# Performance work log

Measured on AMD Instinct MI355X. Metric: run time of the kernel, lower is better.

The kernel has to match this reference:

```python
import jax, jax.numpy as jnp
import numpy as np

N = 768          # number of atoms
DIM = 3
F = 128          # feature width
N_RBF = 32       # gaussian radial basis size
CUTOFF = 5.0
NUM_CHAINS = 4
T_IN_K = 300.0
TTIME = 20.0
KB = 8.617330337217213e-05   # Boltzmann constant, eV/K (ASE units.kB)
BOX = 24.8                   # box side so that ~26 neighbors/atom within cutoff
GAMMA = 1.0 / (CUTOFF / N_RBF) ** 2  # RBF width


def setup_inputs() -> dict:
    key = jax.random.key(0)
    ks = jax.random.split(key, 12)
    q = jax.random.uniform(ks[0], (N, DIM), dtype=jnp.float32) * BOX
    v = jax.random.normal(ks[1], (N, DIM), dtype=jnp.float32) * 0.01
    p_eta = jax.random.normal(ks[2], (NUM_CHAINS,), dtype=jnp.float32) * 0.1
    mass = jax.random.uniform(ks[3], (N,), dtype=jnp.float32, minval=1.0, maxval=20.0)
    atomic_numbers = jax.random.randint(ks[4], (N,), 0, 100, dtype=jnp.int32)
    embed = jax.random.normal(ks[5], (100, F), dtype=jnp.float32) * 0.1
    W1 = jax.random.normal(ks[6], (N_RBF, F), dtype=jnp.float32) / np.sqrt(N_RBF)
    b1 = jnp.zeros((F,), dtype=jnp.float32)
    W2 = jax.random.normal(ks[7], (F, F), dtype=jnp.float32) / np.sqrt(F)
    b2 = jnp.zeros((F,), dtype=jnp.float32)
    W3 = jax.random.normal(ks[8], (F, F), dtype=jnp.float32) / np.sqrt(F)
    w_out = jax.random.normal(ks[9], (F,), dtype=jnp.float32) / np.sqrt(F)
    return dict(v=v, q=q, p_eta=p_eta, mass=mass, embed=embed, W1=W1, b1=b1,
                W2=W2, b2=b2, W3=W3, w_out=w_out, atomic_numbers=atomic_numbers)


def _energy(q, atomic_numbers, embed, W1, b1, W2, b2, W3, w_out):
    """SchNet-style cutoff-graph potential energy (scalar)."""
    h = embed[atomic_numbers]                                   # [N,F]
    disp = q[:, None, :] - q[None, :, :]                        # [N,N,3]
    d2 = jnp.sum(disp * disp, axis=-1)                          # [N,N]
    eye = jnp.eye(N, dtype=bool)
    mask = (d2 < CUTOFF ** 2) & (~eye)                          # cutoff neighbor list (dense mask)
    d = jnp.sqrt(jnp.where(mask, d2, 1.0))                      # safe sqrt off-graph
    centers = jnp.linspace(0.0, CUTOFF, N_RBF, dtype=q.dtype)
    rbf = jnp.exp(-GAMMA * (d[..., None] - centers) ** 2)       # [N,N,n_rbf]
    filt = jax.nn.relu(rbf @ W1 + b1) @ W2 + b2                 # [N,N,F]
    filt = jnp.where(mask[..., None], filt, 0.0)
    m = jnp.einsum('ijf,jf->if', filt, h)                       # message aggregation
    h = h + jax.nn.relu(m @ W3)
    return jnp.sum(h @ w_out)


def reference(v, q, p_eta, mass, embed, W1, b1, W2, b2, W3, w_out, atomic_numbers):
    kT = T_IN_K * KB
    n_dof = N * DIM
    target_ke = 0.5 * n_dof * kT
    Q = 2.0 * jnp.array([n_dof * kT * TTIME ** 2] + [kT * TTIME ** 2] * (NUM_CHAINS - 1),
                        dtype=v.dtype)
    p = v * mass[:, None]                                       # momenta
    current_ke = 0.5 * jnp.sum(p * p / mass[:, None])
    # f = -dE/dq (torch: -results['energy_grad'])
    f = -jax.grad(_energy)(q, atomic_numbers, embed, W1, b1, W2, b2, W3, w_out)
    coupled_forces = (p_eta[0] * p.reshape(-1) / Q[0]).reshape(-1, 3)
    dvdt = (f - coupled_forces) / mass[:, None]
    dpeta_first = 2.0 * (current_ke - target_ke) - p_eta[0] * p_eta[1] / Q[1]
    dpeta_mid = p_eta[:-2] ** 2 / Q[:-2] - kT - p_eta[1:-1] * p_eta[2:] / Q[2:]
    dpeta_last = p_eta[-2] ** 2 / Q[-2] - kT
    dpeta_dt = jnp.concatenate([dpeta_first[None], dpeta_mid, dpeta_last[None]])
    return (dvdt, v, dpeta_dt)
```

## Files before the change

### kernel.cpp

```cpp
#include <hip/hip_runtime.h>
#include <math.h>

#define N_ATOMS 768
#define FD 128
#define NRBF 32
#define MAXN 64
#define NTHREADS 512
#define TST 136
#define RSTU 40

constexpr float  CUT2   = 25.0f;
constexpr float  GAMMA_ = 40.96f;
constexpr float  CSTEP  = 5.0f / 31.0f;
constexpr double KB_D   = 8.617330337217213e-05;
constexpr double KT_D   = 300.0 * KB_D;
constexpr float  KT_F   = (float)KT_D;
constexpr float  TARGET_KE = (float)(0.5 * 2304.0 * KT_D);
constexpr float  Q0_F   = (float)(2.0 * 2304.0 * KT_D * 400.0);
constexpr float  QI_F   = (float)(2.0 * KT_D * 400.0);

#define DVDT_OFF 0
#define V_OFF    (3 * N_ATOMS)
#define PETA_OFF (6 * N_ATOMS)

using short8v = __attribute__((ext_vector_type(8))) short;
using f32x4   = __attribute__((ext_vector_type(4))) float;

#define MFMA_B16 __builtin_amdgcn_mfma_f32_16x16x32_bf16

__device__ __forceinline__ unsigned short f2bf(float x) {
    unsigned int u = __float_as_uint(x);
    u += 0x7FFF + ((u >> 16) & 1);
    return (unsigned short)(u >> 16);
}
__device__ __forceinline__ float bf2f(unsigned short h) {
    return __uint_as_float(((unsigned int)h) << 16);
}


__global__ __launch_bounds__(256) void prep_kernel(
    const int* __restrict__ z, const float* __restrict__ embed,
    const float* __restrict__ W1, const float* __restrict__ W2,
    const float* __restrict__ W3,
    float* __restrict__ h, float* __restrict__ W3T,
    unsigned short* __restrict__ w1fh, unsigned short* __restrict__ w1fl,
    unsigned short* __restrict__ w2fh, unsigned short* __restrict__ w2fl,
    unsigned short* __restrict__ w2bh, unsigned short* __restrict__ w2bl,
    float* __restrict__ f_acc)
{
    int g = blockIdx.x * 256 + threadIdx.x;
    if (g < N_ATOMS * FD) h[g] = embed[z[g >> 7] * FD + (g & 127)];
    if (g < FD * FD) {
        int r = g >> 7, c = g & 127;
        float w = W2[g];
        unsigned short hb = f2bf(w);
        unsigned short lb = f2bf(w - bf2f(hb));
        w2bh[g] = hb;
        w2bl[g] = lb;
        w2fh[c * FD + r] = hb;
        w2fl[c * FD + r] = lb;
        W3T[c * FD + r] = W3[g];
        if (g < NRBF * FD) {
            float w1v = W1[g];
            unsigned short h1 = f2bf(w1v);
            w1fh[c * NRBF + r] = h1;
            w1fl[c * NRBF + r] = f2bf(w1v - bf2f(h1));
        }
    }
    if (g < 3 * N_ATOMS) f_acc[g] = 0.f;
}

__global__ __launch_bounds__(NTHREADS) void atom_kernel(
    const float* __restrict__ q,
    const unsigned short* __restrict__ w1fh, const unsigned short* __restrict__ w1fl,
    const float* __restrict__ b1,
    const unsigned short* __restrict__ w2fh, const unsigned short* __restrict__ w2fl,
    const unsigned short* __restrict__ w2bh, const unsigned short* __restrict__ w2bl,
    const float* __restrict__ b2, const float* __restrict__ h,
    const float* __restrict__ W3, const float* __restrict__ W3T,
    const float* __restrict__ wout,
    float* __restrict__ f_acc)
{
    __shared__ int   nj[MAXN];
    __shared__ float nd[MAXN], ndx[MAXN], ndy[MAXN], ndz[MAXN];
    __shared__ int   cnt_s;
    __shared__ __align__(16) unsigned short poolR[2 * MAXN * RSTU];
    __shared__ __align__(16) unsigned short poolA[2 * MAXN * TST];
    __shared__ float mrow[FD], gb[FD], mbrow[FD];
    __shared__ float sred[8 * MAXN];

    unsigned short* rbf_h  = poolR;
    unsigned short* rbf_l  = poolR + MAXN * RSTU;
    unsigned short* crbf_h = poolR;
    unsigned short* crbf_l = poolR + MAXN * RSTU;
    unsigned short* a1h  = poolA;
    unsigned short* a1l  = poolA + MAXN * TST;
    unsigned short* ts_h = poolA;
    unsigned short* ts_l = poolA + MAXN * TST;

    int i = blockIdx.x, t = threadIdx.x;
    int wid = t >> 6, lane = t & 63;
    int lr = lane & 15, lg = lane >> 4;
    int c0 = wid * 16 + lr;

    if (t == 0) cnt_s = 0;
    __syncthreads();

    short8v w1h_r = *(const short8v*)(w1fh + c0 * NRBF + lg * 8);
    short8v w1l_r = *(const short8v*)(w1fl + c0 * NRBF + lg * 8);
    short8v w2f_h[4], w2f_l[4];
#pragma unroll
    for (int ks = 0; ks < 4; ks++) {
        int kb = ks * 32 + lg * 8;
        w2f_h[ks] = *(const short8v*)(w2fh + c0 * FD + kb);
        w2f_l[ks] = *(const short8v*)(w2fl + c0 * FD + kb);
    }
    float bb0  = b1[c0];
    float b2c0 = b2[c0];

    float qx = q[i*3], qy = q[i*3+1], qz = q[i*3+2];
    for (int j = t; j < N_ATOMS; j += NTHREADS) {
        if (j == i) continue;
        float dx = qx - q[j*3], dy = qy - q[j*3+1], dz = qz - q[j*3+2];
        float d2 = dx*dx + dy*dy + dz*dz;
        if (d2 < CUT2) {
            int p = atomicAdd(&cnt_s, 1);
            if (p < MAXN) { nj[p] = j; nd[p] = sqrtf(d2);
                            ndx[p] = dx; ndy[p] = dy; ndz[p] = dz; }
        }
    }
    __syncthreads();
    int cnt = min(cnt_s, MAXN);
    if (cnt == 0) return;
    int ntl = (cnt + 15) >> 4;

    float macc0 = 0.f;
    unsigned int mk = 0;

    float4 hj0[2];
#pragma unroll
    for (int e = 0; e < 2; e++) {
        int idx = t + e * NTHREADS;
        int p = idx >> 5, c4g = (idx & 31) * 4;
        hj0[e] = (p < cnt) ? *(const float4*)(h + nj[p] * FD + c4g)
                           : make_float4(0.f, 0.f, 0.f, 0.f);
    }

    for (int e = 0; e < ntl; e++) {
        int idx = t + e * NTHREADS;
        int p = idx >> 5, k = idx & 31;
        float d = (p < cnt) ? nd[p] : 1.0f;
        float u = d - CSTEP * (float)k;
        float r = __expf(-GAMMA_ * u * u);
        unsigned short hb = f2bf(r);
        rbf_h[p * RSTU + k] = hb;
        rbf_l[p * RSTU + k] = f2bf(r - bf2f(hb));
    }
    __syncthreads();

    for (int tl = 0; tl < ntl; tl++) {
        int rb = tl * 16;
        f32x4 u0 = {bb0, bb0, bb0, bb0};
        short8v rh = *(const short8v*)(rbf_h + (rb + lr) * RSTU + lg * 8);
        short8v rl = *(const short8v*)(rbf_l + (rb + lr) * RSTU + lg * 8);
        u0 = MFMA_B16(rh, w1h_r, u0, 0,0,0);
        u0 = MFMA_B16(rh, w1l_r, u0, 0,0,0);
        u0 = MFMA_B16(rl, w1h_r, u0, 0,0,0);
#pragma unroll
        for (int r = 0; r < 4; r++) {
            int p = rb + lg * 4 + r;
            if (u0[r] > 0.f) mk |= 1u << (4 * tl + r);
            float v = fmaxf(u0[r], 0.f);
            unsigned short hb = f2bf(v);
            a1h[p * TST + c0] = hb;
            a1l[p * TST + c0] = f2bf(v - bf2f(hb));
        }
    }
    __syncthreads();

    for (int tl = 0; tl < ntl; tl++) {
        int rb = tl * 16;
        float hv[4];
#pragma unroll
        for (int r = 0; r < 4; r++) {
            int p = rb + lg * 4 + r;
            hv[r] = (p < cnt) ? h[nj[p] * FD + c0] : 0.f;
        }
        f32x4 acc = {0.f, 0.f, 0.f, 0.f};
#pragma unroll
        for (int ks = 0; ks < 4; ks++) {
            int kb = ks * 32 + lg * 8;
            short8v ah = *(const short8v*)(a1h + (rb + lr) * TST + kb);
            short8v al = *(const short8v*)(a1l + (rb + lr) * TST + kb);
            acc = MFMA_B16(ah, w2f_h[ks], acc, 0,0,0);
            acc = MFMA_B16(ah, w2f_l[ks], acc, 0,0,0);
            acc = MFMA_B16(al, w2f_h[ks], acc, 0,0,0);
        }
#pragma unroll
        for (int r = 0; r < 4; r++) macc0 += (acc[r] + b2c0) * hv[r];
    }

    short8v w2b_h[4], w2b_l[4];
#pragma unroll
    for (int ks = 0; ks < 4; ks++) {
        int kb = ks * 32 + lg * 8;
        w2b_h[ks] = *(const short8v*)(w2bh + c0 * FD + kb);
        w2b_l[ks] = *(const short8v*)(w2bl + c0 * FD + kb);
    }

    {
        float r0 = macc0 + __shfl_xor(macc0, 16, 64);
        r0 += __shfl_xor(r0, 32, 64);
        if (lg == 0) mrow[c0] = r0;
    }
    __syncthreads();

    {
        int f0h = lg * 32;
        float g = 0.f;
#pragma unroll
        for (int f4 = 0; f4 < 32; f4 += 4) {
            float4 w  = *(const float4*)(W3T + c0 * FD + f0h + f4);
            float4 mr = *(const float4*)(mrow + f0h + f4);
            g += mr.x*w.x + mr.y*w.y + mr.z*w.z + mr.w*w.w;
        }
        g += __shfl_xor(g, 16, 64);
        g += __shfl_xor(g, 32, 64);
        if (lg == 0) gb[c0] = (g > 0.f) ? wout[c0] : 0.f;
    }
    __syncthreads();
    {
        int f0h = lg * 32;
        float mb = 0.f;
#pragma unroll
        for (int f4 = 0; f4 < 32; f4 += 4) {
            float4 w  = *(const float4*)(W3 + c0 * FD + f0h + f4);
            float4 gv = *(const float4*)(gb + f0h + f4);
            mb += gv.x*w.x + gv.y*w.y + gv.z*w.z + gv.w*w.w;
        }
        mb += __shfl_xor(mb, 16, 64);
        mb += __shfl_xor(mb, 32, 64);
        if (lg == 0) mbrow[c0] = mb;
    }
    __syncthreads();

    for (int e = 0; e < ntl; e++) {
        int idx = t + e * NTHREADS;
        int p = idx >> 5, k = idx & 31;
        float d = (p < cnt) ? nd[p] : 1.0f;
        float u = d - CSTEP * (float)k;
        float r = __expf(-GAMMA_ * u * u);
        float cd = -2.f * GAMMA_ * u * r;
        unsigned short hc = f2bf(cd);
        crbf_h[p * RSTU + k] = hc;
        crbf_l[p * RSTU + k] = f2bf(cd - bf2f(hc));
    }
    for (int e = 0; e < ntl; e++) {
        int idx = t + e * NTHREADS;
        int p = idx >> 5, c4g = (idx & 31) * 4;
        ushort4 hv = {0,0,0,0}, lv = {0,0,0,0};
        if (p < cnt) {
            float4 mb4 = *(const float4*)(mbrow + c4g);
            float4 hj4 = (e < 2) ? hj0[e]
                                 : *(const float4*)(h + nj[p] * FD + c4g);
            float v0 = mb4.x*hj4.x, v1 = mb4.y*hj4.y;
            float v2 = mb4.z*hj4.z, v3 = mb4.w*hj4.w;
            hv.x = f2bf(v0); lv.x = f2bf(v0 - bf2f(hv.x));
            hv.y = f2bf(v1); lv.y = f2bf(v1 - bf2f(hv.y));
            hv.z = f2bf(v2); lv.z = f2bf(v2 - bf2f(hv.z));
            hv.w = f2bf(v3); lv.w = f2bf(v3 - bf2f(hv.w));
        }
        *(ushort4*)(ts_h + p * TST + c4g) = hv;
        *(ushort4*)(ts_l + p * TST + c4g) = lv;
    }
    __syncthreads();

    for (int tl = 0; tl < ntl; tl++) {
        int rb = tl * 16;
        f32x4 ef = {0.f, 0.f, 0.f, 0.f};
        {
            short8v ch = *(const short8v*)(crbf_h + (rb + lr) * RSTU + lg * 8);
            short8v cl = *(const short8v*)(crbf_l + (rb + lr) * RSTU + lg * 8);
            ef = MFMA_B16(ch, w1h_r, ef, 0,0,0);
            ef = MFMA_B16(ch, w1l_r, ef, 0,0,0);
            ef = MFMA_B16(cl, w1h_r, ef, 0,0,0);
        }
        unsigned int mt = (mk >> (4 * tl)) & 0xFu;
#pragma unroll
        for (int r = 0; r < 4; r++)
            ef[r] = (mt & (1u << r)) ? ef[r] : 0.f;

        f32x4 acc = {0.f, 0.f, 0.f, 0.f};
#pragma unroll
        for (int ks = 0; ks < 4; ks++) {
            int kb = ks * 32 + lg * 8;
            short8v ah = *(const short8v*)(ts_h + (rb + lr) * TST + kb);
            short8v al = *(const short8v*)(ts_l + (rb + lr) * TST + kb);
            acc = MFMA_B16(ah, w2b_h[ks], acc, 0,0,0);
            acc = MFMA_B16(ah, w2b_l[ks], acc, 0,0,0);
            acc = MFMA_B16(al, w2b_h[ks], acc, 0,0,0);
        }

        float p4[4];
#pragma unroll
        for (int r = 0; r < 4; r++) p4[r] = acc[r] * ef[r];
#pragma unroll
        for (int mask = 1; mask < 16; mask <<= 1) {
#pragma unroll
            for (int e = 0; e < 4; e++) p4[e] += __shfl_xor(p4[e], mask, 64);
        }
        if (lr == 0) {
#pragma unroll
            for (int r = 0; r < 4; r++)
                sred[wid * MAXN + rb + lg * 4 + r] = p4[r];
        }
    }
    __syncthreads();

    float iax = 0.f, iay = 0.f, iaz = 0.f;
    if (t < MAXN && t < cnt) {
        float s = 0.f;
#pragma unroll
        for (int w = 0; w < 8; w++) s += sred[w * MAXN + t];
        float coef = s / nd[t];
        float fx = coef * ndx[t];
        float fy = coef * ndy[t];
        float fz = coef * ndz[t];
        iax = fx; iay = fy; iaz = fz;
        atomicAdd(f_acc + nj[t]*3 + 0, fx);
        atomicAdd(f_acc + nj[t]*3 + 1, fy);
        atomicAdd(f_acc + nj[t]*3 + 2, fz);
    }

    if (t < MAXN) {
#pragma unroll
        for (int mask = 1; mask < 64; mask <<= 1) {
            iax += __shfl_xor(iax, mask, 64);
            iay += __shfl_xor(iay, mask, 64);
            iaz += __shfl_xor(iaz, mask, 64);
        }
        if (t == 0) {
            atomicAdd(f_acc + i*3 + 0, -iax);
            atomicAdd(f_acc + i*3 + 1, -iay);
            atomicAdd(f_acc + i*3 + 2, -iaz);
        }
    }
}

__global__ __launch_bounds__(256) void fin_kernel(
    const float* __restrict__ v, const float* __restrict__ mass,
    const float* __restrict__ p_eta, const float* __restrict__ f_acc,
    float* __restrict__ out)
{
    __shared__ float red[256];
    int t = threadIdx.x;
    float ke = 0.f;
    float c = p_eta[0] / Q0_F;
    for (int idx = t; idx < 3 * N_ATOMS; idx += 256) {
        int a = idx / 3;
        float vv = v[idx], mi = mass[a];
        out[DVDT_OFF + idx] = (f_acc[idx] - c * vv * mi) / mi;
        out[V_OFF + idx] = vv;
        ke += 0.5f * mi * vv * vv;
    }
    red[t] = ke;
    __syncthreads();
    for (int s = 128; s > 0; s >>= 1) {
        if (t < s) red[t] += red[t + s];
        __syncthreads();
    }
    if (t == 0) {
        float k0 = red[0];
        float e0 = p_eta[0], e1 = p_eta[1], e2 = p_eta[2], e3 = p_eta[3];
        out[PETA_OFF + 0] = 2.f * (k0 - TARGET_KE) - e0 * e1 / QI_F;
        out[PETA_OFF + 1] = e0 * e0 / Q0_F - KT_F - e1 * e2 / QI_F;
        out[PETA_OFF + 2] = e1 * e1 / QI_F - KT_F - e2 * e3 / QI_F;
        out[PETA_OFF + 3] = e2 * e2 / QI_F - KT_F;
    }
}

extern "C" void kernel_launch(void* const* d_in, const int* in_sizes, int n_in,
                              void* d_out, int out_size, void* d_ws, size_t ws_size,
                              hipStream_t stream)
{
    const float* v     = (const float*)d_in[0];
    const float* q     = (const float*)d_in[1];
    const float* p_eta = (const float*)d_in[2];
    const float* mass  = (const float*)d_in[3];
    const float* embed = (const float*)d_in[4];
    const float* W1    = (const float*)d_in[5];
    const float* b1    = (const float*)d_in[6];
    const float* W2    = (const float*)d_in[7];
    const float* b2    = (const float*)d_in[8];
    const float* W3    = (const float*)d_in[9];
    const float* wout  = (const float*)d_in[10];
    const int*   z     = (const int*)d_in[11];
    float* out = (float*)d_out;

    float* h     = (float*)d_ws;
    float* W3T   = h + N_ATOMS * FD;
    float* f_acc = W3T + FD * FD;
    unsigned short* w2bh = (unsigned short*)(f_acc + 3 * N_ATOMS);
    unsigned short* w2bl = w2bh + FD * FD;
    unsigned short* w2fh = w2bl + FD * FD;
    unsigned short* w2fl = w2fh + FD * FD;
    unsigned short* w1fh = w2fl + FD * FD;
    unsigned short* w1fl = w1fh + NRBF * FD;

    prep_kernel<<<384, 256, 0, stream>>>(z, embed, W1, W2, W3, h, W3T,
                                         w1fh, w1fl, w2fh, w2fl, w2bh, w2bl,
                                         f_acc);
    atom_kernel<<<N_ATOMS, NTHREADS, 0, stream>>>(q, w1fh, w1fl, b1, w2fh, w2fl,
                                                  w2bh, w2bl, b2, h, W3, W3T, wout,
                                                  f_acc);
    fin_kernel<<<1, 256, 0, stream>>>(v, mass, p_eta, f_acc, out);
}
```

Measured before the change: 122.9 us.

## Fold weight preprocessing into atom kernel and drop prep launch

Removes the separate prep kernel that built the gathered embedding table, transposed W3 and bf16 hi/lo splits of W1/W2. The atom kernel now reads raw fp32 weights and embeddings, splitting them into bf16 hi/lo in registers and staging atomic numbers in shared memory. The f_acc zeroing becomes a memset. This saves a kernel launch and a global round trip, but every block repeats the conversion work, does strided uncoalesced loads of W1, W2 and W3, and uses more shared memory.

```diff
diff --git a/kernel.cpp b/kernel.cpp
--- a/kernel.cpp
+++ b/kernel.cpp
@@ -38,52 +38,18 @@
 }
 
 
-__global__ __launch_bounds__(256) void prep_kernel(
-    const int* __restrict__ z, const float* __restrict__ embed,
-    const float* __restrict__ W1, const float* __restrict__ W2,
-    const float* __restrict__ W3,
-    float* __restrict__ h, float* __restrict__ W3T,
-    unsigned short* __restrict__ w1fh, unsigned short* __restrict__ w1fl,
-    unsigned short* __restrict__ w2fh, unsigned short* __restrict__ w2fl,
-    unsigned short* __restrict__ w2bh, unsigned short* __restrict__ w2bl,
-    float* __restrict__ f_acc)
-{
-    int g = blockIdx.x * 256 + threadIdx.x;
-    if (g < N_ATOMS * FD) h[g] = embed[z[g >> 7] * FD + (g & 127)];
-    if (g < FD * FD) {
-        int r = g >> 7, c = g & 127;
-        float w = W2[g];
-        unsigned short hb = f2bf(w);
-        unsigned short lb = f2bf(w - bf2f(hb));
-        w2bh[g] = hb;
-        w2bl[g] = lb;
-        w2fh[c * FD + r] = hb;
-        w2fl[c * FD + r] = lb;
-        W3T[c * FD + r] = W3[g];
-        if (g < NRBF * FD) {
-            float w1v = W1[g];
-            unsigned short h1 = f2bf(w1v);
-            w1fh[c * NRBF + r] = h1;
-            w1fl[c * NRBF + r] = f2bf(w1v - bf2f(h1));
-        }
-    }
-    if (g < 3 * N_ATOMS) f_acc[g] = 0.f;
-}
-
 __global__ __launch_bounds__(NTHREADS) void atom_kernel(
     const float* __restrict__ q,
-    const unsigned short* __restrict__ w1fh, const unsigned short* __restrict__ w1fl,
-    const float* __restrict__ b1,
-    const unsigned short* __restrict__ w2fh, const unsigned short* __restrict__ w2fl,
-    const unsigned short* __restrict__ w2bh, const unsigned short* __restrict__ w2bl,
-    const float* __restrict__ b2, const float* __restrict__ h,
-    const float* __restrict__ W3, const float* __restrict__ W3T,
-    const float* __restrict__ wout,
+    const float* __restrict__ W1, const float* __restrict__ b1,
+    const float* __restrict__ W2, const float* __restrict__ b2,
+    const float* __restrict__ embed, const int* __restrict__ z,
+    const float* __restrict__ W3, const float* __restrict__ wout,
     float* __restrict__ f_acc)
 {
     __shared__ int   nj[MAXN];
     __shared__ float nd[MAXN], ndx[MAXN], ndy[MAXN], ndz[MAXN];
     __shared__ int   cnt_s;
+    __shared__ int   z_s[N_ATOMS];
     __shared__ __align__(16) unsigned short poolR[2 * MAXN * RSTU];
     __shared__ __align__(16) unsigned short poolA[2 * MAXN * TST];
     __shared__ float mrow[FD], gb[FD], mbrow[FD];
@@ -106,20 +72,21 @@
     if (t == 0) cnt_s = 0;
     __syncthreads();
 
-    short8v w1h_r = *(const short8v*)(w1fh + c0 * NRBF + lg * 8);
-    short8v w1l_r = *(const short8v*)(w1fl + c0 * NRBF + lg * 8);
-    short8v w2f_h[4], w2f_l[4];
-#pragma unroll
-    for (int ks = 0; ks < 4; ks++) {
-        int kb = ks * 32 + lg * 8;
-        w2f_h[ks] = *(const short8v*)(w2fh + c0 * FD + kb);
-        w2f_l[ks] = *(const short8v*)(w2fl + c0 * FD + kb);
-    }
+    float w1f32[8], w2ff32[4][8];
+#pragma unroll
+    for (int e = 0; e < 8; e++)
+        w1f32[e] = W1[(lg * 8 + e) * FD + c0];
+#pragma unroll
+    for (int ks = 0; ks < 4; ks++)
+#pragma unroll
+        for (int e = 0; e < 8; e++)
+            w2ff32[ks][e] = W2[(ks * 32 + lg * 8 + e) * FD + c0];
     float bb0  = b1[c0];
     float b2c0 = b2[c0];
 
     float qx = q[i*3], qy = q[i*3+1], qz = q[i*3+2];
     for (int j = t; j < N_ATOMS; j += NTHREADS) {
+        z_s[j] = z[j];
         if (j == i) continue;
         float dx = qx - q[j*3], dy = qy - q[j*3+1], dz = qz - q[j*3+2];
         float d2 = dx*dx + dy*dy + dz*dz;
@@ -134,6 +101,22 @@
     if (cnt == 0) return;
     int ntl = (cnt + 15) >> 4;
 
+    short8v w1h_r, w1l_r, w2f_h[4], w2f_l[4];
+#pragma unroll
+    for (int e = 0; e < 8; e++) {
+        unsigned short hb = f2bf(w1f32[e]);
+        w1h_r[e] = (short)hb;
+        w1l_r[e] = (short)f2bf(w1f32[e] - bf2f(hb));
+    }
+#pragma unroll
+    for (int ks = 0; ks < 4; ks++)
+#pragma unroll
+        for (int e = 0; e < 8; e++) {
+            unsigned short hb = f2bf(w2ff32[ks][e]);
+            w2f_h[ks][e] = (short)hb;
+            w2f_l[ks][e] = (short)f2bf(w2ff32[ks][e] - bf2f(hb));
+        }
+
     float macc0 = 0.f;
     unsigned int mk = 0;
 
@@ -142,8 +125,9 @@
     for (int e = 0; e < 2; e++) {
         int idx = t + e * NTHREADS;
         int p = idx >> 5, c4g = (idx & 31) * 4;
-        hj0[e] = (p < cnt) ? *(const float4*)(h + nj[p] * FD + c4g)
-                           : make_float4(0.f, 0.f, 0.f, 0.f);
+        hj0[e] = (p < cnt)
+            ? *(const float4*)(embed + z_s[nj[p]] * FD + c4g)
+            : make_float4(0.f, 0.f, 0.f, 0.f);
     }
 
     for (int e = 0; e < ntl; e++) {
@@ -184,7 +168,7 @@
 #pragma unroll
         for (int r = 0; r < 4; r++) {
             int p = rb + lg * 4 + r;
-            hv[r] = (p < cnt) ? h[nj[p] * FD + c0] : 0.f;
+            hv[r] = (p < cnt) ? embed[z_s[nj[p]] * FD + c0] : 0.f;
         }
         f32x4 acc = {0.f, 0.f, 0.f, 0.f};
 #pragma unroll
@@ -204,8 +188,15 @@
 #pragma unroll
     for (int ks = 0; ks < 4; ks++) {
         int kb = ks * 32 + lg * 8;
-        w2b_h[ks] = *(const short8v*)(w2bh + c0 * FD + kb);
-        w2b_l[ks] = *(const short8v*)(w2bl + c0 * FD + kb);
+        float4 a = *(const float4*)(W2 + c0 * FD + kb);
+        float4 b = *(const float4*)(W2 + c0 * FD + kb + 4);
+        float vv[8] = {a.x, a.y, a.z, a.w, b.x, b.y, b.z, b.w};
+#pragma unroll
+        for (int e = 0; e < 8; e++) {
+            unsigned short hb = f2bf(vv[e]);
+            w2b_h[ks][e] = (short)hb;
+            w2b_l[ks][e] = (short)f2bf(vv[e] - bf2f(hb));
+        }
     }
 
     {
@@ -218,12 +209,9 @@
     {
         int f0h = lg * 32;
         float g = 0.f;
-#pragma unroll
-        for (int f4 = 0; f4 < 32; f4 += 4) {
-            float4 w  = *(const float4*)(W3T + c0 * FD + f0h + f4);
-            float4 mr = *(const float4*)(mrow + f0h + f4);
-            g += mr.x*w.x + mr.y*w.y + mr.z*w.z + mr.w*w.w;
-        }
+#pragma unroll 8
+        for (int f = f0h; f < f0h + 32; f++)
+            g += mrow[f] * W3[f * FD + c0];
         g += __shfl_xor(g, 16, 64);
         g += __shfl_xor(g, 32, 64);
         if (lg == 0) gb[c0] = (g > 0.f) ? wout[c0] : 0.f;
@@ -262,7 +250,7 @@
         if (p < cnt) {
             float4 mb4 = *(const float4*)(mbrow + c4g);
             float4 hj4 = (e < 2) ? hj0[e]
-                                 : *(const float4*)(h + nj[p] * FD + c4g);
+                : *(const float4*)(embed + z_s[nj[p]] * FD + c4g);
             float v0 = mb4.x*hj4.x, v1 = mb4.y*hj4.y;
             float v2 = mb4.z*hj4.z, v3 = mb4.w*hj4.w;
             hv.x = f2bf(v0); lv.x = f2bf(v0 - bf2f(hv.x));
@@ -397,21 +385,11 @@
     const int*   z     = (const int*)d_in[11];
     float* out = (float*)d_out;
 
-    float* h     = (float*)d_ws;
-    float* W3T   = h + N_ATOMS * FD;
-    float* f_acc = W3T + FD * FD;
-    unsigned short* w2bh = (unsigned short*)(f_acc + 3 * N_ATOMS);
-    unsigned short* w2bl = w2bh + FD * FD;
-    unsigned short* w2fh = w2bl + FD * FD;
-    unsigned short* w2fl = w2fh + FD * FD;
-    unsigned short* w1fh = w2fl + FD * FD;
-    unsigned short* w1fl = w1fh + NRBF * FD;
-
-    prep_kernel<<<384, 256, 0, stream>>>(z, embed, W1, W2, W3, h, W3T,
-                                         w1fh, w1fl, w2fh, w2fl, w2bh, w2bl,
-                                         f_acc);
-    atom_kernel<<<N_ATOMS, NTHREADS, 0, stream>>>(q, w1fh, w1fl, b1, w2fh, w2fl,
-                                                  w2bh, w2bl, b2, h, W3, W3T, wout,
-                                                  f_acc);
+    float* f_acc = (float*)d_ws;
+
+    hipMemsetAsync(f_acc, 0, 3 * N_ATOMS * sizeof(float), stream);
+
+    atom_kernel<<<N_ATOMS, NTHREADS, 0, stream>>>(q, W1, b1, W2, b2,
+                                                  embed, z, W3, wout, f_acc);
     fin_kernel<<<1, 256, 0, stream>>>(v, mass, p_eta, f_acc, out);
 }
```

New measurement: 117.9 us. -4.1%, faster.
